# Optimization experiments

Measured on AMD Instinct MI355X. Metric: run time of the kernel, lower is better.

The kernel has to match this reference:

```python
import jax, jax.numpy as jnp
import numpy as np

N_NODES = 100000
N_EDGES = 1600000
IN_DIM = 128
OUT_DIM = 32
N_HEADS = 4


def setup_inputs() -> dict:
    key = jax.random.key(0)
    k1, k2, k3, k4, k5 = jax.random.split(key, 5)
    x = jax.random.normal(k1, (N_NODES, IN_DIM), dtype=jnp.float32)
    edge_index = jax.random.randint(k2, (2, N_EDGES), 0, N_NODES, dtype=jnp.int64)
    # torch nn.Linear weight layout: [out_features, in_features]
    W = jax.random.normal(k3, (OUT_DIM * N_HEADS, IN_DIM), dtype=jnp.float32) * (1.0 / np.sqrt(IN_DIM))
    a_left = jax.random.normal(k4, (N_HEADS, OUT_DIM), dtype=jnp.float32) * 0.01
    a_right = jax.random.normal(k5, (N_HEADS, OUT_DIM), dtype=jnp.float32) * 0.01
    return {"x": x, "edge_index": edge_index, "W": W, "a_left": a_left, "a_right": a_right}


def reference(x, edge_index, W, a_left, a_right):
    N = x.shape[0]
    H, D = a_left.shape
    # h: [N, H, D]
    h = (x @ W.T).reshape(N, H, D)
    src = edge_index[0]
    dst = edge_index[1]
    h_src = h[src]                                   # [E, H, D] gather
    h_dst = h[dst]                                   # [E, H, D] gather
    e = jnp.einsum('ehd,hd->eh', h_src, a_left) + jnp.einsum('ehd,hd->eh', h_dst, a_right)
    e = jax.nn.leaky_relu(e, negative_slope=0.2)
    e_exp = jnp.exp(e)                               # faithful: no max-subtraction, as in source
    denom = jax.ops.segment_sum(e_exp, dst, num_segments=N)   # [N, H]
    alpha = e_exp / (denom[dst] + 1e-8)              # [E, H]
    weighted = h_src * alpha[:, :, None]             # [E, H, D]
    out = jax.ops.segment_sum(weighted, dst, num_segments=N)  # [N, H, D]
    return out.reshape(N, H * D)                     # concat=True
```

## Files before the change

kernel.cpp:

```cpp
#include <hip/hip_runtime.h>
#include <hip/hip_bf16.h>


constexpr int IN_DIM = 128;
constexpr int HD     = 128;
constexpr int CSHIFT = 10;
constexpr int CCAP   = 17408;
constexpr int CPAD   = 16;

typedef float f32x4 __attribute__((ext_vector_type(4)));
typedef short short8 __attribute__((ext_vector_type(8)));

__device__ __forceinline__ unsigned short f2bf(float f) {
  __hip_bfloat16 b = __float2bfloat16(f);
  return *(unsigned short*)&b;
}
__device__ __forceinline__ float bfl(unsigned u) { return __uint_as_float(u << 16); }
__device__ __forceinline__ float bfh(unsigned u) { return __uint_as_float(u & 0xffff0000u); }

__global__ __launch_bounds__(256)
void gemm_k(const float* __restrict__ x, const float* __restrict__ W,
            const float* __restrict__ a_left, const float* __restrict__ a_right,
            unsigned int* __restrict__ hb,
            float* __restrict__ el, float* __restrict__ er,
            int N) {
  __shared__ __align__(16) char xs[32768];
  const int tid  = threadIdx.x;
  const int lane = tid & 63;
  const int wv   = tid >> 6;
  const int lcol = lane & 15;
  const int lk   = lane >> 4;
  const int n0   = blockIdx.x * 64;

  short8 Bh[2][4], Bl[2][4];
#pragma unroll
  for (int ct = 0; ct < 2; ++ct) {
    int col = wv * 32 + ct * 16 + lcol;
#pragma unroll
    for (int ks = 0; ks < 4; ++ks) {
      int kb = ks * 32 + lk * 8;
      const float* wp = &W[col * IN_DIM + kb];
      float4 wa = *(const float4*)wp;
      float4 wb = *(const float4*)(wp + 4);
      float wf[8] = {wa.x, wa.y, wa.z, wa.w, wb.x, wb.y, wb.z, wb.w};
      short8 uh, ul;
#pragma unroll
      for (int j = 0; j < 8; ++j) {
        unsigned short hs = f2bf(wf[j]);
        float hf = __uint_as_float((unsigned)hs << 16);
        uh[j] = (short)hs;
        ul[j] = (short)f2bf(wf[j] - hf);
      }
      Bh[ct][ks] = uh;  Bl[ct][ks] = ul;
    }
  }

#pragma unroll
  for (int i = 0; i < 8; ++i) {
    int f  = tid + 256 * i;
    int r  = f >> 5;
    int c4 = f & 31;
    int node = n0 + r;
    float4 v = make_float4(0.f, 0.f, 0.f, 0.f);
    if (node < N) v = *(const float4*)&x[(size_t)node * IN_DIM + c4 * 4];
    float vf[4] = {v.x, v.y, v.z, v.w};
    unsigned short hs[4], ls[4];
#pragma unroll
    for (int j = 0; j < 4; ++j) {
      hs[j] = f2bf(vf[j]);
      float hf = __uint_as_float((unsigned)hs[j] << 16);
      ls[j] = f2bf(vf[j] - hf);
    }
    int sw = (c4 * 8) ^ ((r & 7) << 4);
    uint2 ph = make_uint2((unsigned)hs[0] | ((unsigned)hs[1] << 16),
                          (unsigned)hs[2] | ((unsigned)hs[3] << 16));
    uint2 pl = make_uint2((unsigned)ls[0] | ((unsigned)ls[1] << 16),
                          (unsigned)ls[2] | ((unsigned)ls[3] << 16));
    *(uint2*)&xs[r * 256 + sw]         = ph;
    *(uint2*)&xs[16384 + r * 256 + sw] = pl;
  }
  __syncthreads();

  f32x4 acc[4][2];
#pragma unroll
  for (int rt = 0; rt < 4; ++rt)
#pragma unroll
    for (int ct = 0; ct < 2; ++ct) acc[rt][ct] = (f32x4){0.f, 0.f, 0.f, 0.f};

#pragma unroll
  for (int ks = 0; ks < 4; ++ks) {
#pragma unroll
    for (int rt = 0; rt < 4; ++rt) {
      int row = rt * 16 + lcol;
      int kb  = ks * 64 + lk * 16;
      int ad  = row * 256 + (kb ^ ((row & 7) << 4));
      short8 ah = *(const short8*)&xs[ad];
      short8 al = *(const short8*)&xs[16384 + ad];
#pragma unroll
      for (int ct = 0; ct < 2; ++ct) {
        acc[rt][ct] = __builtin_amdgcn_mfma_f32_16x16x32_bf16(ah, Bh[ct][ks], acc[rt][ct], 0, 0, 0);
        acc[rt][ct] = __builtin_amdgcn_mfma_f32_16x16x32_bf16(ah, Bl[ct][ks], acc[rt][ct], 0, 0, 0);
        acc[rt][ct] = __builtin_amdgcn_mfma_f32_16x16x32_bf16(al, Bh[ct][ks], acc[rt][ct], 0, 0, 0);
      }
    }
  }

  float aL[2], aR[2];
  aL[0] = a_left [wv * 32 + lcol];  aL[1] = a_left [wv * 32 + 16 + lcol];
  aR[0] = a_right[wv * 32 + lcol];  aR[1] = a_right[wv * 32 + 16 + lcol];

#pragma unroll
  for (int rt = 0; rt < 4; ++rt) {
    float pl[4] = {0.f, 0.f, 0.f, 0.f}, pr[4] = {0.f, 0.f, 0.f, 0.f};
#pragma unroll
    for (int ct = 0; ct < 2; ++ct) {
      float av[4] = {acc[rt][ct][0], acc[rt][ct][1], acc[rt][ct][2], acc[rt][ct][3]};
      float pt[4];
#pragma unroll
      for (int r = 0; r < 4; ++r) pt[r] = __shfl_xor(av[r], 1, 64);
      int col = wv * 32 + ct * 16 + lcol;
      int nb  = n0 + rt * 16 + lk * 4;
      if (!(lane & 1)) {
#pragma unroll
        for (int r = 0; r < 4; ++r) {
          int node = nb + r;
          if (node < N)
            hb[(size_t)node * 64 + (col >> 1)] =
                (unsigned)f2bf(av[r]) | ((unsigned)f2bf(pt[r]) << 16);
        }
      }
#pragma unroll
      for (int r = 0; r < 4; ++r) { pl[r] += av[r] * aL[ct]; pr[r] += av[r] * aR[ct]; }
    }
#pragma unroll
    for (int m = 1; m < 16; m <<= 1)
#pragma unroll
      for (int r = 0; r < 4; ++r) {
        pl[r] += __shfl_xor(pl[r], m, 64);
        pr[r] += __shfl_xor(pr[r], m, 64);
      }
    if (lcol == 0) {
#pragma unroll
      for (int r = 0; r < 4; ++r) {
        int node = n0 + rt * 16 + lk * 4 + r;
        if (node < N) { el[node * 4 + wv] = pl[r]; er[node * 4 + wv] = pr[r]; }
      }
    }
  }
}

__global__ __launch_bounds__(1024)
void binA_k(const int* __restrict__ ei, int* __restrict__ ccnt,
            unsigned* __restrict__ c1buf, int E, int ncb) {
  __shared__ unsigned staged[8192];
  __shared__ unsigned short sbin[8192];
  __shared__ int hist[128], loff[128], cur[128], gbase[128];
  __shared__ int lws[2];
  const int t = threadIdx.x;
  const int base = blockIdx.x * 8192;

  if (t < 128) hist[t] = 0;
  __syncthreads();

  int src[8], dst[8], bin[8];
#pragma unroll
  for (int i = 0; i < 8; ++i) {
    int e = base + t + 1024 * i;
    if (e < E) {
      src[i] = ei[e];
      dst[i] = ei[E + e];
      bin[i] = dst[i] >> CSHIFT;
      atomicAdd(&hist[bin[i]], 1);
    } else bin[i] = -1;
  }
  __syncthreads();

  int v = 0, s = 0;
  if (t < 128) {
    v = hist[t]; s = v;
#pragma unroll
    for (int d = 1; d < 64; d <<= 1) {
      int u = __shfl_up(s, d, 64);
      if ((t & 63) >= d) s += u;
    }
    if ((t & 63) == 63) lws[t >> 6] = s;
  }
  __syncthreads();
  if (t < 128) {
    int prefix = (t >= 64) ? lws[0] : 0;
    int excl = prefix + s - v;
    loff[t] = excl;
    cur[t]  = excl;
    gbase[t] = (t < ncb && v > 0) ? atomicAdd(&ccnt[t * CPAD], v) : 0;
  }
  __syncthreads();

#pragma unroll
  for (int i = 0; i < 8; ++i) {
    if (bin[i] >= 0) {
      int p = atomicAdd(&cur[bin[i]], 1);
      staged[p] = (unsigned)src[i] | ((unsigned)(dst[i] & 1023) << 17);
      sbin[p]   = (unsigned short)bin[i];
    }
  }
  __syncthreads();

  const int tot = loff[127] + hist[127];
  for (int j = t; j < tot; j += 1024) {
    int b = sbin[j];
    int pos = gbase[b] + (j - loff[b]);
    if (pos < CCAP) c1buf[(size_t)b * CCAP + pos] = staged[j];
  }
}

__global__ __launch_bounds__(1024)
void binB_k(const unsigned* __restrict__ c1buf, const int* __restrict__ ccnt,
            int* __restrict__ offsets, int* __restrict__ csr,
            int N, int ncb, int E) {
  __shared__ int hist[1024];
  __shared__ int wsum[16];
  __shared__ int lws2[2];
  __shared__ int sgb;
  const int b = blockIdx.x, t = threadIdx.x;
  int m = ccnt[b * CPAD];
  if (m > CCAP) m = CCAP;
  hist[t] = 0;

  int cv = 0, cs = 0;
  if (t < 128) {
    cv = (t < ncb) ? ccnt[t * CPAD] : 0;
    cs = cv;
#pragma unroll
    for (int d = 1; d < 64; d <<= 1) {
      int u = __shfl_up(cs, d, 64);
      if ((t & 63) >= d) cs += u;
    }
    if ((t & 63) == 63) lws2[t >> 6] = cs;
  }
  if (t == 0 && b == 0) offsets[N] = E;
  __syncthreads();
  if (t < 128) {
    int prefix = (t >= 64) ? lws2[0] : 0;
    if (t == b) sgb = prefix + cs - cv;
  }
  __syncthreads();
  const int gb = sgb;

  const unsigned* bp = c1buf + (size_t)b * CCAP;
  for (int i = t; i < m; i += 1024) atomicAdd(&hist[bp[i] >> 17], 1);
  __syncthreads();
  int v = hist[t], s = v;
#pragma unroll
  for (int d = 1; d < 64; d <<= 1) {
    int u = __shfl_up(s, d, 64);
    if ((t & 63) >= d) s += u;
  }
  if ((t & 63) == 63) wsum[t >> 6] = s;
  __syncthreads();
  int prefix = 0;
  for (int w = 0; w < (t >> 6); ++w) prefix += wsum[w];
  int excl = prefix + s - v;
  int node = (b << CSHIFT) + t;
  if (node < N) offsets[node] = gb + excl;
  hist[t] = excl;
  __syncthreads();
  for (int i = t; i < m; i += 1024) {
    unsigned u = bp[i];
    int r = atomicAdd(&hist[u >> 17], 1);
    csr[gb + r] = (int)(u & 0x1FFFFu);
  }
}

__global__ __launch_bounds__(256)
void agg_k(const char* __restrict__ hbc, const char* __restrict__ elc,
           const float* __restrict__ er, const int* __restrict__ offsets,
           const int* __restrict__ csr, float* __restrict__ out, int N) {
  const int wid  = (blockIdx.x * blockDim.x + threadIdx.x) >> 6;
  const int lane = threadIdx.x & 63;
  if (wid >= N) return;
  const int start = offsets[wid];
  const int end   = offsets[wid + 1];
  const int q    = lane >> 4;
  const int ql   = lane & 15;
  const int head = ql >> 2;
  const unsigned qoff = (unsigned)(ql << 4);
  const unsigned hoff = (unsigned)(head << 2);
  const float erv = er[wid * 4 + head];

  float a0=0.f,a1=0.f,a2=0.f,a3=0.f,a4=0.f,a5=0.f,a6=0.f,a7=0.f,den=0.f;

  for (int base = start; base < end; base += 64) {
    int lim = end - base; if (lim > 64) lim = 64;
    int ce  = base + lane;
    int creg = __builtin_nontemporal_load(&csr[(ce < end) ? ce : (end - 1)]);

    int i = 0;
    for (; i + 8 <= lim; i += 8) {
      int s0 = __shfl(creg, i + q, 64);
      int s1 = __shfl(creg, i + 4 + q, 64);
      uint4 h0 = *(const uint4*)(hbc + (((unsigned)s0 << 8) + qoff));
      uint4 h1 = *(const uint4*)(hbc + (((unsigned)s1 << 8) + qoff));
      float e0 = *(const float*)(elc + (((unsigned)s0 << 4) + hoff));
      float e1 = *(const float*)(elc + (((unsigned)s1 << 4) + hoff));
      float t0 = e0 + erv; t0 = (t0 > 0.f) ? t0 : 0.2f * t0;
      float t1 = e1 + erv; t1 = (t1 > 0.f) ? t1 : 0.2f * t1;
      float w0 = __expf(t0), w1 = __expf(t1);
      a0 += w0 * bfl(h0.x) + w1 * bfl(h1.x);
      a1 += w0 * bfh(h0.x) + w1 * bfh(h1.x);
      a2 += w0 * bfl(h0.y) + w1 * bfl(h1.y);
      a3 += w0 * bfh(h0.y) + w1 * bfh(h1.y);
      a4 += w0 * bfl(h0.z) + w1 * bfl(h1.z);
      a5 += w0 * bfh(h0.z) + w1 * bfh(h1.z);
      a6 += w0 * bfl(h0.w) + w1 * bfl(h1.w);
      a7 += w0 * bfh(h0.w) + w1 * bfh(h1.w);
      den += w0 + w1;
    }
    if (i < lim) {
      int i0 = i + q, i1 = i + 4 + q;
      int s0 = __shfl(creg, (i0 < lim) ? i0 : 0, 64);
      int s1 = __shfl(creg, (i1 < lim) ? i1 : 0, 64);
      uint4 h0 = *(const uint4*)(hbc + (((unsigned)s0 << 8) + qoff));
      uint4 h1 = *(const uint4*)(hbc + (((unsigned)s1 << 8) + qoff));
      float e0 = *(const float*)(elc + (((unsigned)s0 << 4) + hoff));
      float e1 = *(const float*)(elc + (((unsigned)s1 << 4) + hoff));
      float t0 = e0 + erv; t0 = (t0 > 0.f) ? t0 : 0.2f * t0;
      float t1 = e1 + erv; t1 = (t1 > 0.f) ? t1 : 0.2f * t1;
      float w0 = __expf(t0), w1 = __expf(t1);
      if (i0 >= lim) w0 = 0.f;
      if (i1 >= lim) w1 = 0.f;
      a0 += w0 * bfl(h0.x) + w1 * bfl(h1.x);
      a1 += w0 * bfh(h0.x) + w1 * bfh(h1.x);
      a2 += w0 * bfl(h0.y) + w1 * bfl(h1.y);
      a3 += w0 * bfh(h0.y) + w1 * bfh(h1.y);
      a4 += w0 * bfl(h0.z) + w1 * bfl(h1.z);
      a5 += w0 * bfh(h0.z) + w1 * bfh(h1.z);
      a6 += w0 * bfl(h0.w) + w1 * bfl(h1.w);
      a7 += w0 * bfh(h0.w) + w1 * bfh(h1.w);
      den += w0 + w1;
    }
  }

#pragma unroll
  for (int m = 16; m < 64; m <<= 1) {
    a0 += __shfl_xor(a0, m, 64);  a1 += __shfl_xor(a1, m, 64);
    a2 += __shfl_xor(a2, m, 64);  a3 += __shfl_xor(a3, m, 64);
    a4 += __shfl_xor(a4, m, 64);  a5 += __shfl_xor(a5, m, 64);
    a6 += __shfl_xor(a6, m, 64);  a7 += __shfl_xor(a7, m, 64);
    den += __shfl_xor(den, m, 64);
  }
  if (q == 0) {
    float inv = 1.f / (den + 1e-8f);
    f32x4 o0 = {a0 * inv, a1 * inv, a2 * inv, a3 * inv};
    f32x4 o1 = {a4 * inv, a5 * inv, a6 * inv, a7 * inv};
    __builtin_nontemporal_store(o0, (f32x4*)&out[(size_t)wid * HD + 8 * ql]);
    __builtin_nontemporal_store(o1, (f32x4*)&out[(size_t)wid * HD + 8 * ql + 4]);
  }
}

extern "C" void kernel_launch(void* const* d_in, const int* in_sizes, int n_in,
                              void* d_out, int out_size, void* d_ws, size_t ws_size,
                              hipStream_t stream) {
  const float* x       = (const float*)d_in[0];
  const int*   ei      = (const int*)d_in[1];
  const float* W       = (const float*)d_in[2];
  const float* a_left  = (const float*)d_in[3];
  const float* a_right = (const float*)d_in[4];
  float* out = (float*)d_out;

  const int N = in_sizes[0] / IN_DIM;
  const int E = in_sizes[1] / 2;
  const int NCB = (N + 1023) >> CSHIFT;

  char* p = (char*)d_ws;
  unsigned int* hb = (unsigned int*)p; p += (size_t)N * 64 * sizeof(unsigned int);
  float* el      = (float*)p; p += (size_t)N * 4 * sizeof(float);
  float* er      = (float*)p; p += (size_t)N * 4 * sizeof(float);
  int*   offsets = (int*)p;   p += (size_t)(N + 1) * sizeof(int);
  int*   ccnt    = (int*)p;   p += (size_t)NCB * CPAD * sizeof(int);
  int*   csr     = (int*)p;   p += (size_t)E * sizeof(int);
  unsigned* c1buf = (unsigned*)p; p += (size_t)NCB * CCAP * sizeof(unsigned);

  hipMemsetAsync(ccnt, 0, (size_t)NCB * CPAD * sizeof(int), stream);

  gemm_k<<<(N + 63) / 64, 256, 0, stream>>>(x, W, a_left, a_right, hb, el, er, N);
  binA_k<<<(E + 8191) / 8192, 1024, 0, stream>>>(ei, ccnt, c1buf, E, NCB);
  binB_k<<<NCB, 1024, 0, stream>>>(c1buf, ccnt, offsets, csr, N, NCB, E);
  agg_k<<<(N + 3) / 4, 256, 0, stream>>>((const char*)hb, (const char*)el, er,
                                         offsets, csr, out, N);
}
```

Measured before the change: 238.2 us.

## Restructure CSR binning with global degree counts and smaller coarse bins

The coarse bin width drops from 1024 to 512 nodes and the block size from 1024 to 512 threads. The first pass no longer stages edges in shared memory for coalesced writes. It scatters directly, using positions returned by shared atomics, and also builds a per-node degree histogram with global atomics. The second pass reads those global counts, so its shared-memory histogram pass over each bin is gone and only the scatter remains. The trade is extra global atomics and uncoalesced writes in the first pass against fewer passes and a smaller, higher-occupancy second kernel.

```diff
diff --git a/kernel.cpp b/kernel.cpp
--- a/kernel.cpp
+++ b/kernel.cpp
@@ -4,8 +4,8 @@
 
 constexpr int IN_DIM = 128;
 constexpr int HD     = 128;
-constexpr int CSHIFT = 10;
-constexpr int CCAP   = 17408;
+constexpr int CSHIFT = 9;
+constexpr int CCAP   = 9216;
 constexpr int CPAD   = 16;
 
 typedef float f32x4 __attribute__((ext_vector_type(4)));
@@ -149,125 +149,86 @@
   }
 }
 
-__global__ __launch_bounds__(1024)
-void binA_k(const int* __restrict__ ei, int* __restrict__ ccnt,
-            unsigned* __restrict__ c1buf, int E, int ncb) {
-  __shared__ unsigned staged[8192];
-  __shared__ unsigned short sbin[8192];
-  __shared__ int hist[128], loff[128], cur[128], gbase[128];
-  __shared__ int lws[2];
+__global__ __launch_bounds__(512)
+void binA_k(const int* __restrict__ ei, int* __restrict__ cnt,
+            int* __restrict__ ccnt, unsigned* __restrict__ c1buf,
+            int E, int ncb) {
+  __shared__ int hist[256], gbase[256];
   const int t = threadIdx.x;
-  const int base = blockIdx.x * 8192;
-
-  if (t < 128) hist[t] = 0;
-  __syncthreads();
-
-  int src[8], dst[8], bin[8];
+  const int base = blockIdx.x * 4096;
+  if (t < 256) hist[t] = 0;
+  __syncthreads();
+
+  int bin[8], p[8];
+  unsigned pay[8];
 #pragma unroll
   for (int i = 0; i < 8; ++i) {
-    int e = base + t + 1024 * i;
+    int e = base + t + 512 * i;
     if (e < E) {
-      src[i] = ei[e];
-      dst[i] = ei[E + e];
-      bin[i] = dst[i] >> CSHIFT;
-      atomicAdd(&hist[bin[i]], 1);
+      int s = ei[e];
+      int d = ei[E + e];
+      bin[i] = d >> CSHIFT;
+      pay[i] = (unsigned)s | ((unsigned)(d & 511) << 17);
+      p[i]   = atomicAdd(&hist[bin[i]], 1);
+      atomicAdd(&cnt[d], 1);
     } else bin[i] = -1;
   }
   __syncthreads();
-
-  int v = 0, s = 0;
-  if (t < 128) {
-    v = hist[t]; s = v;
-#pragma unroll
-    for (int d = 1; d < 64; d <<= 1) {
-      int u = __shfl_up(s, d, 64);
-      if ((t & 63) >= d) s += u;
-    }
-    if ((t & 63) == 63) lws[t >> 6] = s;
-  }
-  __syncthreads();
-  if (t < 128) {
-    int prefix = (t >= 64) ? lws[0] : 0;
-    int excl = prefix + s - v;
-    loff[t] = excl;
-    cur[t]  = excl;
-    gbase[t] = (t < ncb && v > 0) ? atomicAdd(&ccnt[t * CPAD], v) : 0;
-  }
-  __syncthreads();
-
+  if (t < 256) {
+    int h = hist[t];
+    gbase[t] = (t < ncb && h > 0) ? atomicAdd(&ccnt[t * CPAD], h) : 0;
+  }
+  __syncthreads();
 #pragma unroll
   for (int i = 0; i < 8; ++i) {
     if (bin[i] >= 0) {
-      int p = atomicAdd(&cur[bin[i]], 1);
-      staged[p] = (unsigned)src[i] | ((unsigned)(dst[i] & 1023) << 17);
-      sbin[p]   = (unsigned short)bin[i];
-    }
-  }
-  __syncthreads();
-
-  const int tot = loff[127] + hist[127];
-  for (int j = t; j < tot; j += 1024) {
-    int b = sbin[j];
-    int pos = gbase[b] + (j - loff[b]);
-    if (pos < CCAP) c1buf[(size_t)b * CCAP + pos] = staged[j];
-  }
-}
-
-__global__ __launch_bounds__(1024)
+      int pos = gbase[bin[i]] + p[i];
+      if (pos < CCAP) c1buf[(size_t)bin[i] * CCAP + pos] = pay[i];
+    }
+  }
+}
+
+__global__ __launch_bounds__(512)
 void binB_k(const unsigned* __restrict__ c1buf, const int* __restrict__ ccnt,
-            int* __restrict__ offsets, int* __restrict__ csr,
-            int N, int ncb, int E) {
-  __shared__ int hist[1024];
-  __shared__ int wsum[16];
-  __shared__ int lws2[2];
+            const int* __restrict__ cnt, int* __restrict__ offsets,
+            int* __restrict__ csr, int N, int ncb, int E) {
+  __shared__ int cur[512];
+  __shared__ int wsA[8], wsB[8];
   __shared__ int sgb;
   const int b = blockIdx.x, t = threadIdx.x;
+  const int w = t >> 6;
+
+  int cv = (t < ncb) ? ccnt[t * CPAD] : 0;
+  int cs = cv;
+  int v  = cnt[(b << CSHIFT) + t];
+  int s  = v;
+#pragma unroll
+  for (int d = 1; d < 64; d <<= 1) {
+    int u1 = __shfl_up(cs, d, 64);
+    int u2 = __shfl_up(s,  d, 64);
+    if ((t & 63) >= d) { cs += u1; s += u2; }
+  }
+  if ((t & 63) == 63) { wsA[w] = cs; wsB[w] = s; }
+  __syncthreads();
+  int cpre = 0, pre = 0;
+  for (int i = 0; i < w; ++i) { cpre += wsA[i]; pre += wsB[i]; }
+  if (t == b) sgb = cpre + cs - cv;
+  __syncthreads();
+  const int gb = sgb;
+  int off = gb + pre + s - v;
+  int node = (b << CSHIFT) + t;
+  if (node < N) offsets[node] = off;
+  cur[t] = off;
+  if (b == 0 && t == 0) offsets[N] = E;
+  __syncthreads();
+
   int m = ccnt[b * CPAD];
   if (m > CCAP) m = CCAP;
-  hist[t] = 0;
-
-  int cv = 0, cs = 0;
-  if (t < 128) {
-    cv = (t < ncb) ? ccnt[t * CPAD] : 0;
-    cs = cv;
-#pragma unroll
-    for (int d = 1; d < 64; d <<= 1) {
-      int u = __shfl_up(cs, d, 64);
-      if ((t & 63) >= d) cs += u;
-    }
-    if ((t & 63) == 63) lws2[t >> 6] = cs;
-  }
-  if (t == 0 && b == 0) offsets[N] = E;
-  __syncthreads();
-  if (t < 128) {
-    int prefix = (t >= 64) ? lws2[0] : 0;
-    if (t == b) sgb = prefix + cs - cv;
-  }
-  __syncthreads();
-  const int gb = sgb;
-
   const unsigned* bp = c1buf + (size_t)b * CCAP;
-  for (int i = t; i < m; i += 1024) atomicAdd(&hist[bp[i] >> 17], 1);
-  __syncthreads();
-  int v = hist[t], s = v;
-#pragma unroll
-  for (int d = 1; d < 64; d <<= 1) {
-    int u = __shfl_up(s, d, 64);
-    if ((t & 63) >= d) s += u;
-  }
-  if ((t & 63) == 63) wsum[t >> 6] = s;
-  __syncthreads();
-  int prefix = 0;
-  for (int w = 0; w < (t >> 6); ++w) prefix += wsum[w];
-  int excl = prefix + s - v;
-  int node = (b << CSHIFT) + t;
-  if (node < N) offsets[node] = gb + excl;
-  hist[t] = excl;
-  __syncthreads();
-  for (int i = t; i < m; i += 1024) {
+  for (int i = t; i < m; i += 512) {
     unsigned u = bp[i];
-    int r = atomicAdd(&hist[u >> 17], 1);
-    csr[gb + r] = (int)(u & 0x1FFFFu);
+    int r = atomicAdd(&cur[u >> 17], 1);
+    csr[r] = (int)(u & 0x1FFFFu);
   }
 }
 
@@ -369,22 +330,24 @@
 
   const int N = in_sizes[0] / IN_DIM;
   const int E = in_sizes[1] / 2;
-  const int NCB = (N + 1023) >> CSHIFT;
+  const int NCB = (N + (1 << CSHIFT) - 1) >> CSHIFT;
+  const int NPAD = NCB << CSHIFT;
 
   char* p = (char*)d_ws;
   unsigned int* hb = (unsigned int*)p; p += (size_t)N * 64 * sizeof(unsigned int);
   float* el      = (float*)p; p += (size_t)N * 4 * sizeof(float);
   float* er      = (float*)p; p += (size_t)N * 4 * sizeof(float);
   int*   offsets = (int*)p;   p += (size_t)(N + 1) * sizeof(int);
-  int*   ccnt    = (int*)p;   p += (size_t)NCB * CPAD * sizeof(int);
+  int*   cnt     = (int*)p;   p += (size_t)NPAD * sizeof(int);
+  int*   ccnt    = (int*)p;   p += (size_t)256 * CPAD * sizeof(int);
   int*   csr     = (int*)p;   p += (size_t)E * sizeof(int);
   unsigned* c1buf = (unsigned*)p; p += (size_t)NCB * CCAP * sizeof(unsigned);
 
-  hipMemsetAsync(ccnt, 0, (size_t)NCB * CPAD * sizeof(int), stream);
+  hipMemsetAsync(cnt, 0, ((size_t)NPAD + 256 * CPAD) * sizeof(int), stream);
 
   gemm_k<<<(N + 63) / 64, 256, 0, stream>>>(x, W, a_left, a_right, hb, el, er, N);
-  binA_k<<<(E + 8191) / 8192, 1024, 0, stream>>>(ei, ccnt, c1buf, E, NCB);
-  binB_k<<<NCB, 1024, 0, stream>>>(c1buf, ccnt, offsets, csr, N, NCB, E);
+  binA_k<<<(E + 4095) / 4096, 512, 0, stream>>>(ei, cnt, ccnt, c1buf, E, NCB);
+  binB_k<<<NCB, 512, 0, stream>>>(c1buf, ccnt, cnt, offsets, csr, N, NCB, E);
   agg_k<<<(N + 3) / 4, 256, 0, stream>>>((const char*)hb, (const char*)el, er,
                                          offsets, csr, out, N);
 }
```

New measurement: 292.7 us. +22.9%, slower.

## Fuse GEMM and edge binning into one heterogeneous kernel with finer buckets

Applied to the files above, without the earlier changes.

The GEMM and the first binning pass now run in a single launch, with blocks interleaved between the two roles so the compute-bound projection overlaps the memory-bound edge bucketing. Bucket granularity drops from 1024 to 512 nodes, so there are more, smaller buckets, and the second pass uses 512-thread blocks. Edge-index loads become nontemporal. This removes one launch and lets the two independent stages share the GPU, at the cost of more global atomics on the bucket counters and smaller binning blocks.

```diff
diff --git a/kernel.cpp b/kernel.cpp
--- a/kernel.cpp
+++ b/kernel.cpp
@@ -4,8 +4,8 @@
 
 constexpr int IN_DIM = 128;
 constexpr int HD     = 128;
-constexpr int CSHIFT = 10;
-constexpr int CCAP   = 17408;
+constexpr int CSHIFT = 9;
+constexpr int CCAP   = 9216;
 constexpr int CPAD   = 16;
 
 typedef float f32x4 __attribute__((ext_vector_type(4)));
@@ -18,19 +18,18 @@
 __device__ __forceinline__ float bfl(unsigned u) { return __uint_as_float(u << 16); }
 __device__ __forceinline__ float bfh(unsigned u) { return __uint_as_float(u & 0xffff0000u); }
 
-__global__ __launch_bounds__(256)
-void gemm_k(const float* __restrict__ x, const float* __restrict__ W,
-            const float* __restrict__ a_left, const float* __restrict__ a_right,
-            unsigned int* __restrict__ hb,
-            float* __restrict__ el, float* __restrict__ er,
-            int N) {
-  __shared__ __align__(16) char xs[32768];
+__device__ __forceinline__
+void gemm_role(char* xs, int gb_idx,
+               const float* __restrict__ x, const float* __restrict__ W,
+               const float* __restrict__ a_left, const float* __restrict__ a_right,
+               unsigned int* __restrict__ hb,
+               float* __restrict__ el, float* __restrict__ er, int N) {
   const int tid  = threadIdx.x;
   const int lane = tid & 63;
   const int wv   = tid >> 6;
   const int lcol = lane & 15;
   const int lk   = lane >> 4;
-  const int n0   = blockIdx.x * 64;
+  const int n0   = gb_idx * 64;
 
   short8 Bh[2][4], Bl[2][4];
 #pragma unroll
@@ -149,85 +148,102 @@
   }
 }
 
-__global__ __launch_bounds__(1024)
-void binA_k(const int* __restrict__ ei, int* __restrict__ ccnt,
-            unsigned* __restrict__ c1buf, int E, int ncb) {
-  __shared__ unsigned staged[8192];
-  __shared__ unsigned short sbin[8192];
-  __shared__ int hist[128], loff[128], cur[128], gbase[128];
-  __shared__ int lws[2];
+__device__ __forceinline__
+void binA_role(char* smem, int ab_idx,
+               const int* __restrict__ ei, int* __restrict__ ccnt,
+               unsigned* __restrict__ c1buf, int E, int ncb) {
+  unsigned*       staged = (unsigned*)smem;
+  unsigned short* sbin   = (unsigned short*)(smem + 8192);
+  int*            hist   = (int*)(smem + 12288);
+  int*            loff   = (int*)(smem + 13312);
+  int*            cur    = (int*)(smem + 14336);
+  int*            gbase  = (int*)(smem + 15360);
+  int*            lws    = (int*)(smem + 16384);
   const int t = threadIdx.x;
-  const int base = blockIdx.x * 8192;
-
-  if (t < 128) hist[t] = 0;
+  const int base = ab_idx * 2048;
+
+  hist[t] = 0;
   __syncthreads();
 
   int src[8], dst[8], bin[8];
 #pragma unroll
   for (int i = 0; i < 8; ++i) {
-    int e = base + t + 1024 * i;
+    int e = base + t + 256 * i;
     if (e < E) {
-      src[i] = ei[e];
-      dst[i] = ei[E + e];
+      src[i] = __builtin_nontemporal_load(&ei[e]);
+      dst[i] = __builtin_nontemporal_load(&ei[E + e]);
       bin[i] = dst[i] >> CSHIFT;
       atomicAdd(&hist[bin[i]], 1);
     } else bin[i] = -1;
   }
   __syncthreads();
 
-  int v = 0, s = 0;
-  if (t < 128) {
-    v = hist[t]; s = v;
-#pragma unroll
-    for (int d = 1; d < 64; d <<= 1) {
-      int u = __shfl_up(s, d, 64);
-      if ((t & 63) >= d) s += u;
-    }
-    if ((t & 63) == 63) lws[t >> 6] = s;
-  }
-  __syncthreads();
-  if (t < 128) {
-    int prefix = (t >= 64) ? lws[0] : 0;
-    int excl = prefix + s - v;
-    loff[t] = excl;
-    cur[t]  = excl;
-    gbase[t] = (t < ncb && v > 0) ? atomicAdd(&ccnt[t * CPAD], v) : 0;
-  }
+  int v = hist[t], s = v;
+#pragma unroll
+  for (int d = 1; d < 64; d <<= 1) {
+    int u = __shfl_up(s, d, 64);
+    if ((t & 63) >= d) s += u;
+  }
+  if ((t & 63) == 63) lws[t >> 6] = s;
+  __syncthreads();
+  int prefix = 0;
+  for (int i = 0; i < (t >> 6); ++i) prefix += lws[i];
+  int excl = prefix + s - v;
+  loff[t] = excl;
+  cur[t]  = excl;
+  gbase[t] = (t < ncb && v > 0) ? atomicAdd(&ccnt[t * CPAD], v) : 0;
   __syncthreads();
 
 #pragma unroll
   for (int i = 0; i < 8; ++i) {
     if (bin[i] >= 0) {
       int p = atomicAdd(&cur[bin[i]], 1);
-      staged[p] = (unsigned)src[i] | ((unsigned)(dst[i] & 1023) << 17);
+      staged[p] = (unsigned)src[i] | ((unsigned)(dst[i] & 511) << 17);
       sbin[p]   = (unsigned short)bin[i];
     }
   }
   __syncthreads();
 
-  const int tot = loff[127] + hist[127];
-  for (int j = t; j < tot; j += 1024) {
+  const int tot = loff[255] + hist[255];
+  for (int j = t; j < tot; j += 256) {
     int b = sbin[j];
     int pos = gbase[b] + (j - loff[b]);
     if (pos < CCAP) c1buf[(size_t)b * CCAP + pos] = staged[j];
   }
 }
 
-__global__ __launch_bounds__(1024)
+__global__ __launch_bounds__(256)
+void fused_k(const float* __restrict__ x, const float* __restrict__ W,
+             const float* __restrict__ a_left, const float* __restrict__ a_right,
+             unsigned int* __restrict__ hb, float* __restrict__ el,
+             float* __restrict__ er, const int* __restrict__ ei,
+             int* __restrict__ ccnt, unsigned* __restrict__ c1buf,
+             int N, int E, int ncb, int nab) {
+  __shared__ __align__(16) char smem[32768];
+  const int k = blockIdx.x;
+  const int twoA = 2 * nab;
+  if (k < twoA && (k & 1)) {
+    binA_role(smem, k >> 1, ei, ccnt, c1buf, E, ncb);
+  } else {
+    int gidx = (k < twoA) ? (k >> 1) : (k - nab);
+    gemm_role(smem, gidx, x, W, a_left, a_right, hb, el, er, N);
+  }
+}
+
+__global__ __launch_bounds__(512)
 void binB_k(const unsigned* __restrict__ c1buf, const int* __restrict__ ccnt,
             int* __restrict__ offsets, int* __restrict__ csr,
             int N, int ncb, int E) {
-  __shared__ int hist[1024];
-  __shared__ int wsum[16];
-  __shared__ int lws2[2];
+  __shared__ int hist[512];
+  __shared__ int wsum[8];
+  __shared__ int lws2[4];
   __shared__ int sgb;
   const int b = blockIdx.x, t = threadIdx.x;
-  int m = ccnt[b * CPAD];
-  if (m > CCAP) m = CCAP;
+
   hist[t] = 0;
 
   int cv = 0, cs = 0;
-  if (t < 128) {
+  if (t < 256) {
     cv = (t < ncb) ? ccnt[t * CPAD] : 0;
     cs = cv;
 #pragma unroll
@@ -239,16 +255,20 @@
   }
   if (t == 0 && b == 0) offsets[N] = E;
   __syncthreads();
-  if (t < 128) {
-    int prefix = (t >= 64) ? lws2[0] : 0;
-    if (t == b) sgb = prefix + cs - cv;
+  if (t < 256) {
+    int cpre = 0;
+    for (int i = 0; i < (t >> 6); ++i) cpre += lws2[i];
+    if (t == b) sgb = cpre + cs - cv;
   }
   __syncthreads();
   const int gb = sgb;
 
+  int m = ccnt[b * CPAD];
+  if (m > CCAP) m = CCAP;
   const unsigned* bp = c1buf + (size_t)b * CCAP;
-  for (int i = t; i < m; i += 1024) atomicAdd(&hist[bp[i] >> 17], 1);
-  __syncthreads();
+  for (int i = t; i < m; i += 512) atomicAdd(&hist[bp[i] >> 17], 1);
+  __syncthreads();
+
   int v = hist[t], s = v;
 #pragma unroll
   for (int d = 1; d < 64; d <<= 1) {
@@ -264,7 +284,8 @@
   if (node < N) offsets[node] = gb + excl;
   hist[t] = excl;
   __syncthreads();
-  for (int i = t; i < m; i += 1024) {
+
+  for (int i = t; i < m; i += 512) {
     unsigned u = bp[i];
     int r = atomicAdd(&hist[u >> 17], 1);
     csr[gb + r] = (int)(u & 0x1FFFFu);
@@ -369,22 +390,24 @@
 
   const int N = in_sizes[0] / IN_DIM;
   const int E = in_sizes[1] / 2;
-  const int NCB = (N + 1023) >> CSHIFT;
+  const int NCB = (N + (1 << CSHIFT) - 1) >> CSHIFT;
+  const int GB  = (N + 63) / 64;
+  const int AB  = (E + 2047) / 2048;
 
   char* p = (char*)d_ws;
   unsigned int* hb = (unsigned int*)p; p += (size_t)N * 64 * sizeof(unsigned int);
   float* el      = (float*)p; p += (size_t)N * 4 * sizeof(float);
   float* er      = (float*)p; p += (size_t)N * 4 * sizeof(float);
   int*   offsets = (int*)p;   p += (size_t)(N + 1) * sizeof(int);
-  int*   ccnt    = (int*)p;   p += (size_t)NCB * CPAD * sizeof(int);
+  int*   ccnt    = (int*)p;   p += (size_t)256 * CPAD * sizeof(int);
   int*   csr     = (int*)p;   p += (size_t)E * sizeof(int);
   unsigned* c1buf = (unsigned*)p; p += (size_t)NCB * CCAP * sizeof(unsigned);
 
-  hipMemsetAsync(ccnt, 0, (size_t)NCB * CPAD * sizeof(int), stream);
-
-  gemm_k<<<(N + 63) / 64, 256, 0, stream>>>(x, W, a_left, a_right, hb, el, er, N);
-  binA_k<<<(E + 8191) / 8192, 1024, 0, stream>>>(ei, ccnt, c1buf, E, NCB);
-  binB_k<<<NCB, 1024, 0, stream>>>(c1buf, ccnt, offsets, csr, N, NCB, E);
+  hipMemsetAsync(ccnt, 0, (size_t)256 * CPAD * sizeof(int), stream);
+
+  fused_k<<<GB + AB, 256, 0, stream>>>(x, W, a_left, a_right, hb, el, er,
+                                       ei, ccnt, c1buf, N, E, NCB, AB);
+  binB_k<<<NCB, 512, 0, stream>>>(c1buf, ccnt, offsets, csr, N, NCB, E);
   agg_k<<<(N + 3) / 4, 256, 0, stream>>>((const char*)hb, (const char*)el, er,
                                          offsets, csr, out, N);
 }
```

New measurement: 234.4 us. No clear change (-1.6%).
